# Performance work log

Hardware: AMD Instinct MI355X
Metric: run time of the kernel (lower is better)

The kernel has to match this reference:

```python
import jax, jax.numpy as jnp
import numpy as np

G, B, T, D, U = 3, 32, 1024, 512, 512  # branches, batch, time, feat dim, units

def setup_inputs() -> dict:
    key = jax.random.key(0)
    ks = jax.random.split(key, 8)
    s = 0.02
    return {
        "query": jax.random.normal(ks[0], (G, B, D), jnp.float32),
        "values": jax.random.normal(ks[1], (G, B, T, D), jnp.float32),
        "W1": jax.random.normal(ks[2], (G, D, U), jnp.float32) * s,
        "b1": jnp.zeros((G, U), jnp.float32),
        "W2": jax.random.normal(ks[3], (G, D, U), jnp.float32) * s,
        "b2": jnp.zeros((G, U), jnp.float32),
        "V": jax.random.normal(ks[4], (G, U), jnp.float32) * s,
        "bV": jnp.zeros((G,), jnp.float32),
    }

def reference(query, values, W1, b1, W2, b2, V, bV):
    # query: [G,B,D], values: [G,B,T,D]; G=3 independent additive-attention branches.
    qp = jnp.einsum('gbd,gdu->gbu', query, W1) + b1[:, None, :]          # [G,B,U]
    vp = jnp.einsum('gbtd,gdu->gbtu', values, W2) + b2[:, None, None, :]  # [G,B,T,U]
    feat = jnp.tanh(qp[:, :, None, :] + vp)                               # [G,B,T,U]
    score = jnp.einsum('gbtu,gu->gbt', feat, V) + bV[:, None, None]       # [G,B,T]
    weights = jax.nn.softmax(score, axis=2)                               # softmax over time
    context = jnp.einsum('gbt,gbtd->gbd', weights, values)                # [G,B,D]
    return context, weights[..., None]  # matches tf.stack outputs: [3,B,D], [3,B,T,1]
```

## Files before the change

### kernel.cpp

```cpp
#include <hip/hip_runtime.h>
#include <cstdint>
#include <cstddef>

#define NG 3
#define NB 32
#define NT 1024
#define ND 512
#define NU 512

typedef __bf16 bf16x8 __attribute__((ext_vector_type(8)));
typedef float  f32x16 __attribute__((ext_vector_type(16)));

static __device__ __forceinline__ unsigned int f2bf(float f) {
    union { float f; unsigned int u; } v; v.f = f;
    return (v.u + 0x7FFFu + ((v.u >> 16) & 1u)) >> 16;
}

static __device__ __forceinline__ unsigned int cvt_pk_bf16(float lo, float hi) {
    unsigned int r;
    asm("v_cvt_pk_bf16_f32 %0, %1, %2" : "=v"(r) : "v"(lo), "v"(hi));
    return r;
}

static __device__ __forceinline__ bf16x8 ld_bf16x8(const char* base, int off) {
    return __builtin_bit_cast(bf16x8, *(const uint4*)(base + off));
}

#define AS1(p) ((const __attribute__((address_space(1))) void*)(p))
#define AS3(p) ((__attribute__((address_space(3))) void*)(p))

__global__ __launch_bounds__(256) void prep_qb_kernel(
    const float* __restrict__ query, const float* __restrict__ W1,
    const float* __restrict__ b1, const float* __restrict__ b2,
    float* __restrict__ qb)
{
    __shared__ float qs[NB][ND];
    const int g  = blockIdx.x >> 3;
    const int uc = blockIdx.x & 7;
    const int tid = threadIdx.x;

    const float4* qsrc = (const float4*)(query + (size_t)g * NB * ND);
    #pragma unroll
    for (int i = 0; i < 16; ++i)
        ((float4*)&qs[0][0])[tid + i * 256] = qsrc[tid + i * 256];
    __syncthreads();

    const int u  = uc * 64 + (tid & 63);
    const int b0 = tid >> 6;
    float acc[8] = {};
    const float* w1col = W1 + (size_t)g * ND * NU + u;
    for (int d = 0; d < ND; ++d) {
        float w = w1col[(size_t)d * NU];
        #pragma unroll
        for (int j = 0; j < 8; ++j)
            acc[j] = fmaf(qs[b0 + 4 * j][d], w, acc[j]);
    }
    const float bias = b1[g * NU + u] + b2[g * NU + u];
    #pragma unroll
    for (int j = 0; j < 8; ++j)
        qb[((size_t)g * NB + (b0 + 4 * j)) * NU + u] = acc[j] + bias;
}

__global__ __launch_bounds__(256) void prep_w2t_kernel(
    const float* __restrict__ W2, char* __restrict__ w2t)
{
    __shared__ float tile[64][65];
    const int g  = blockIdx.x >> 6;
    const int tb = blockIdx.x & 63;
    const int d0 = (tb >> 3) * 64;
    const int u0 = (tb & 7) * 64;
    const int tx = threadIdx.x & 63;
    const int ty = threadIdx.x >> 6;

    const float* src = W2 + (size_t)g * ND * NU;
    #pragma unroll
    for (int k = 0; k < 16; ++k) {
        int r = ty + 4 * k;
        tile[r][tx] = src[(size_t)(d0 + r) * NU + (u0 + tx)];
    }
    __syncthreads();
    #pragma unroll
    for (int k = 0; k < 16; ++k) {
        int ul = ty + 4 * k;
        int u  = u0 + ul;
        int d  = d0 + tx;
        unsigned short h = (unsigned short)f2bf(tile[tx][ul]);
        int nb2 = u >> 8, up = u & 255, ksd = d >> 6, kp = d & 63;
        size_t off = ((size_t)((((g << 1) + nb2) << 3) + ksd) << 15)
                   + (size_t)((up << 7) + (((kp << 1) ^ ((up & 7) << 4))));
        *(unsigned short*)(w2t + off) = h;
    }
}

__global__ __launch_bounds__(512, 2) void score_kernel(
    const float* __restrict__ values, const char* __restrict__ w2t,
    const float* __restrict__ qbg, const float* __restrict__ Vvec,
    float* __restrict__ part0, float* __restrict__ part1)
{
    __shared__ char Abuf[2][32768];
    __shared__ char Bbuf[2][32768];
    __shared__ float qbs[256];
    __shared__ float Vs[256];
    __shared__ float spart[4][256];

    const int blk  = blockIdx.x;
    const int g    = blk >> 8;
    const int rr   = blk & 255;
    const int mt   = rr >> 1;
    const int nb   = rr & 1;
    const int b    = mt >> 2;
    const int t0   = (mt & 3) << 8;
    const int tid  = threadIdx.x;
    const int lane = tid & 63;
    const int wave = tid >> 6;
    const int wm   = wave >> 2;
    const int wn   = wave & 3;
    const int rl   = lane & 31;
    const int hi   = lane >> 5;

    const char* bimg = w2t + ((size_t)((((g << 1) + nb) << 3)) << 15);

    if (wave < 4) {
        const float* qsrc = qbg + (((size_t)(g * NB + b)) << 9) + (nb << 8) + (wave << 6) + lane;
        __builtin_amdgcn_global_load_lds(AS1(qsrc), AS3(&qbs[(wave << 6) + lane]), 4, 0, 0);
    } else {
        const float* vsrc = Vvec + (g << 9) + (nb << 8) + ((wave - 4) << 6) + lane;
        __builtin_amdgcn_global_load_lds(AS1(vsrc), AS3(&Vs[((wave - 4) << 6) + lane]), 4, 0, 0);
    }

    auto stageB = [&](int ks, char* dst) {
        const char* src = bimg + ((size_t)ks << 15) + (wave << 12) + (lane << 4);
        char* d = dst + (wave << 12) + (lane << 4);
        #pragma unroll
        for (int i = 0; i < 4; ++i)
            __builtin_amdgcn_global_load_lds(AS1(src + (i << 10)), AS3(d + (i << 10)), 16, 0, 0);
    };

    const int arow  = tid >> 1;
    const int ahalf = tid & 1;
    const float* aptr = values
        + (((size_t)((g * NB + b) * NT + t0 + arow)) << 9) + (ahalf << 5);
    const int awswz = (arow & 7) << 4;

    float4 av[8];
    auto loadA = [&](int ks) {
        const float4* p4 = (const float4*)(aptr + (ks << 6));
        #pragma unroll
        for (int i = 0; i < 8; ++i) av[i] = p4[i];
    };
    auto writeA = [&](char* dst) {
        char* base = dst + (arow << 7);
        #pragma unroll
        for (int q = 0; q < 4; ++q) {
            uint4 w;
            w.x = cvt_pk_bf16(av[2*q].x,   av[2*q].y);
            w.y = cvt_pk_bf16(av[2*q].z,   av[2*q].w);
            w.z = cvt_pk_bf16(av[2*q+1].x, av[2*q+1].y);
            w.w = cvt_pk_bf16(av[2*q+1].z, av[2*q+1].w);
            *(uint4*)(base + (((ahalf << 6) + (q << 4)) ^ awswz)) = w;
        }
    };

    const int lswz = (rl & 7) << 4;
    int koff[4];
    #pragma unroll
    for (int kf = 0; kf < 4; ++kf) koff[kf] = ((kf << 5) + (hi << 4)) ^ lswz;
    const int abase = (((wm << 7) + rl) << 7);
    const int bbase = (((wn << 6) + rl) << 7);

    f32x16 acc[4][2];
    #pragma unroll
    for (int mf = 0; mf < 4; ++mf) {
        acc[mf][0] = (f32x16)(0.0f);
        acc[mf][1] = (f32x16)(0.0f);
    }

    char* Ac = Abuf[0]; char* An = Abuf[1];
    char* Bc = Bbuf[0]; char* Bn = Bbuf[1];

    stageB(0, Bc);
    loadA(0);
    asm volatile("s_waitcnt vmcnt(0) lgkmcnt(0)" ::: "memory");
    writeA(Ac);
    asm volatile("s_waitcnt lgkmcnt(0)" ::: "memory");
    __builtin_amdgcn_s_barrier();

    #pragma unroll 1
    for (int ks = 0; ks < 8; ++ks) {
        if (ks < 7) {
            stageB(ks + 1, Bn);
            loadA(ks + 1);
        }
        __builtin_amdgcn_s_setprio(1);
        #pragma unroll
        for (int kf = 0; kf < 4; ++kf) {
            bf16x8 a0 = ld_bf16x8(Ac, abase         + koff[kf]);
            bf16x8 a1 = ld_bf16x8(Ac, abase +  4096 + koff[kf]);
            bf16x8 a2 = ld_bf16x8(Ac, abase +  8192 + koff[kf]);
            bf16x8 a3 = ld_bf16x8(Ac, abase + 12288 + koff[kf]);
            bf16x8 b0 = ld_bf16x8(Bc, bbase         + koff[kf]);
            bf16x8 b1 = ld_bf16x8(Bc, bbase +  4096 + koff[kf]);
            acc[0][0] = __builtin_amdgcn_mfma_f32_32x32x16_bf16(a0, b0, acc[0][0], 0, 0, 0);
            acc[0][1] = __builtin_amdgcn_mfma_f32_32x32x16_bf16(a0, b1, acc[0][1], 0, 0, 0);
            acc[1][0] = __builtin_amdgcn_mfma_f32_32x32x16_bf16(a1, b0, acc[1][0], 0, 0, 0);
            acc[1][1] = __builtin_amdgcn_mfma_f32_32x32x16_bf16(a1, b1, acc[1][1], 0, 0, 0);
            acc[2][0] = __builtin_amdgcn_mfma_f32_32x32x16_bf16(a2, b0, acc[2][0], 0, 0, 0);
            acc[2][1] = __builtin_amdgcn_mfma_f32_32x32x16_bf16(a2, b1, acc[2][1], 0, 0, 0);
            acc[3][0] = __builtin_amdgcn_mfma_f32_32x32x16_bf16(a3, b0, acc[3][0], 0, 0, 0);
            acc[3][1] = __builtin_amdgcn_mfma_f32_32x32x16_bf16(a3, b1, acc[3][1], 0, 0, 0);
        }
        __builtin_amdgcn_s_setprio(0);
        if (ks < 7) {
            asm volatile("s_waitcnt vmcnt(0)" ::: "memory");
            writeA(An);
            asm volatile("s_waitcnt lgkmcnt(0)" ::: "memory");
            __builtin_amdgcn_s_barrier();
            char* t1 = Ac; Ac = An; An = t1;
            char* t2 = Bc; Bc = Bn; Bn = t2;
        }
    }

    const float qv0 = qbs[(wn << 6) + rl];
    const float qv1 = qbs[(wn << 6) + 32 + rl];
    const float vv0 = Vs[(wn << 6) + rl];
    const float vv1 = Vs[(wn << 6) + 32 + rl];
    const float CL = 2.8853900817779268f;
    #pragma unroll
    for (int mf = 0; mf < 4; ++mf) {
        float p[16];
        #pragma unroll
        for (int r2 = 0; r2 < 16; ++r2) {
            float x0 = acc[mf][0][r2] + qv0;
            float x1 = acc[mf][1][r2] + qv1;
            float e0 = exp2f(CL * x0);
            float e1 = exp2f(CL * x1);
            float th0 = 1.f - 2.f * __builtin_amdgcn_rcpf(e0 + 1.f);
            float th1 = 1.f - 2.f * __builtin_amdgcn_rcpf(e1 + 1.f);
            p[r2] = fmaf(th1, vv1, th0 * vv0);
        }
        #pragma unroll
        for (int r2 = 0; r2 < 16; ++r2) {
            float v = p[r2];
            v += __shfl_xor(v, 1);
            v += __shfl_xor(v, 2);
            v += __shfl_xor(v, 4);
            v += __shfl_xor(v, 8);
            v += __shfl_xor(v, 16);
            p[r2] = v;
        }
        if (rl == 0) {
            #pragma unroll
            for (int r2 = 0; r2 < 16; ++r2)
                spart[wn][(wm << 7) + (mf << 5) + (r2 & 3) + 8 * (r2 >> 2) + 4 * hi] = p[r2];
        }
    }
    __syncthreads();
    if (tid < 256) {
        float s = spart[0][tid] + spart[1][tid] + spart[2][tid] + spart[3][tid];
        float* dst = nb ? part1 : part0;
        dst[(((size_t)(g * NB + b)) << 10) + t0 + tid] = s;
    }
}

__global__ __launch_bounds__(256) void finish_kernel(
    const float* __restrict__ part0, const float* __restrict__ part1,
    const float* __restrict__ bV, const float* __restrict__ values,
    float* __restrict__ out_ctx, float* __restrict__ out_w)
{
    __shared__ float sl[NT];
    __shared__ float red[16];
    __shared__ float cred[4][128];
    const int blk   = blockIdx.x;
    const int gb    = blk >> 2;
    const int slice = blk & 3;
    const int tid = threadIdx.x;
    const int lane = tid & 63, wid = tid >> 6;
    const float bv = bV[gb >> 5];

    float s[4];
    #pragma unroll
    for (int j = 0; j < 4; ++j) {
        int idx = (int)((size_t)gb * NT) + tid + 256 * j;
        s[j] = part0[idx] + part1[idx] + bv;
    }

    float m = fmaxf(fmaxf(s[0], s[1]), fmaxf(s[2], s[3]));
    #pragma unroll
    for (int mask = 32; mask; mask >>= 1) m = fmaxf(m, __shfl_xor(m, mask));
    if (lane == 0) red[wid] = m;
    __syncthreads();
    const float gm = fmaxf(fmaxf(red[0], red[1]), fmaxf(red[2], red[3]));

    float e[4], ps = 0.f;
    #pragma unroll
    for (int j = 0; j < 4; ++j) { e[j] = __expf(s[j] - gm); ps += e[j]; }
    #pragma unroll
    for (int mask = 32; mask; mask >>= 1) ps += __shfl_xor(ps, mask);
    if (lane == 0) red[8 + wid] = ps;
    __syncthreads();
    const float inv = 1.f / (red[8] + red[9] + red[10] + red[11]);

    #pragma unroll
    for (int j = 0; j < 4; ++j) {
        float w = e[j] * inv;
        sl[tid + 256 * j] = w;
        if (slice == 0) out_w[(size_t)gb * NT + tid + 256 * j] = w;
    }
    __syncthreads();

    const int dp = tid & 63;
    const int tg = tid >> 6;
    const float* vbase = values + (size_t)gb * NT * ND + slice * 128 + dp * 2;
    float ax = 0.f, ay = 0.f;
    #pragma unroll 4
    for (int t = tg; t < NT; t += 4) {
        float2 v = *(const float2*)(vbase + (size_t)t * ND);
        float w = sl[t];
        ax = fmaf(w, v.x, ax);
        ay = fmaf(w, v.y, ay);
    }
    cred[tg][dp * 2]     = ax;
    cred[tg][dp * 2 + 1] = ay;
    __syncthreads();
    if (tid < 128) {
        float r = cred[0][tid] + cred[1][tid] + cred[2][tid] + cred[3][tid];
        out_ctx[(size_t)gb * ND + slice * 128 + tid] = r;
    }
}

extern "C" void kernel_launch(void* const* d_in, const int* in_sizes, int n_in,
                              void* d_out, int out_size, void* d_ws, size_t ws_size,
                              hipStream_t stream)
{
    (void)in_sizes; (void)n_in; (void)out_size; (void)ws_size;
    const float* query  = (const float*)d_in[0];
    const float* values = (const float*)d_in[1];
    const float* W1     = (const float*)d_in[2];
    const float* b1     = (const float*)d_in[3];
    const float* W2     = (const float*)d_in[4];
    const float* b2     = (const float*)d_in[5];
    const float* Vv     = (const float*)d_in[6];
    const float* bV     = (const float*)d_in[7];

    float* out_ctx = (float*)d_out;
    float* out_w   = out_ctx + (size_t)NG * NB * ND;

    float* qb    = (float*)d_ws;
    float* part0 = qb + (size_t)NG * NB * NU;
    float* part1 = part0 + (size_t)NG * NB * NT;
    char*  w2t   = (char*)(part1 + (size_t)NG * NB * NT);

    prep_qb_kernel <<<NG * 8,   256, 0, stream>>>(query, W1, b1, b2, qb);
    prep_w2t_kernel<<<NG * 64,  256, 0, stream>>>(W2, w2t);
    score_kernel   <<<NG * 256, 512, 0, stream>>>(values, w2t, qb, Vv, part0, part1);
    finish_kernel  <<<NG * NB * 4, 256, 0, stream>>>(part0, part1, bV, values, out_ctx, out_w);
}
```

Before: 177.7 us.

## Restructure score GEMM main loop into barrier-synchronized phases with deeper A prefetch

Replaces the per-k-step loop with a manually unrolled two-step body split into four phases per k-step. Each phase interleaves one slice of global loads (B staging, half of the A register prefetch, or the A conversion write) with one MFMA cluster, fenced by barriers and sched_barriers. A register prefetch now runs two k-steps ahead using two register sets with partial vmcnt waits, aiming to hide global latency and spread LDS traffic. In exchange it adds more barriers per k-step and raises register pressure under the launch bound of two blocks.

```diff
diff --git a/kernel.cpp b/kernel.cpp
--- a/kernel.cpp
+++ b/kernel.cpp
@@ -92,13 +92,82 @@
     }
 }
 
+#define STAGEB(N_, DST_) do {                                                 \
+    const char* _src = bimg + ((size_t)(N_) << 15) + (wave << 12) + (lane << 4); \
+    char* _d = (DST_) + (wave << 12) + (lane << 4);                           \
+    _Pragma("unroll")                                                         \
+    for (int _i = 0; _i < 4; ++_i)                                            \
+        __builtin_amdgcn_global_load_lds(AS1(_src + (_i << 10)),              \
+                                         AS3(_d + (_i << 10)), 16, 0, 0);     \
+} while (0)
+
+#define LOADA_H(AV_, N_, H_) do {                                             \
+    const float4* _p = (const float4*)(aptr + ((N_) << 6)) + ((H_) << 2);     \
+    _Pragma("unroll")                                                         \
+    for (int _i = 0; _i < 4; ++_i) (AV_)[((H_) << 2) + _i] = _p[_i];          \
+} while (0)
+
+#define WRITEA(AV_, DST_) do {                                                \
+    char* _b = (DST_) + (arow << 7);                                          \
+    _Pragma("unroll")                                                         \
+    for (int _q = 0; _q < 4; ++_q) {                                          \
+        uint4 _w;                                                             \
+        _w.x = cvt_pk_bf16((AV_)[2*_q].x,   (AV_)[2*_q].y);                   \
+        _w.y = cvt_pk_bf16((AV_)[2*_q].z,   (AV_)[2*_q].w);                   \
+        _w.z = cvt_pk_bf16((AV_)[2*_q+1].x, (AV_)[2*_q+1].y);                 \
+        _w.w = cvt_pk_bf16((AV_)[2*_q+1].z, (AV_)[2*_q+1].w);                 \
+        *(uint4*)(_b + (((ahalf << 6) + (_q << 4)) ^ awswz)) = _w;            \
+    }                                                                         \
+} while (0)
+
+#define MFMA8(A0_,A1_,A2_,A3_,B0_,B1_) do {                                   \
+    acc[0][0] = __builtin_amdgcn_mfma_f32_32x32x16_bf16(A0_, B0_, acc[0][0], 0, 0, 0); \
+    acc[0][1] = __builtin_amdgcn_mfma_f32_32x32x16_bf16(A0_, B1_, acc[0][1], 0, 0, 0); \
+    acc[1][0] = __builtin_amdgcn_mfma_f32_32x32x16_bf16(A1_, B0_, acc[1][0], 0, 0, 0); \
+    acc[1][1] = __builtin_amdgcn_mfma_f32_32x32x16_bf16(A1_, B1_, acc[1][1], 0, 0, 0); \
+    acc[2][0] = __builtin_amdgcn_mfma_f32_32x32x16_bf16(A2_, B0_, acc[2][0], 0, 0, 0); \
+    acc[2][1] = __builtin_amdgcn_mfma_f32_32x32x16_bf16(A2_, B1_, acc[2][1], 0, 0, 0); \
+    acc[3][0] = __builtin_amdgcn_mfma_f32_32x32x16_bf16(A3_, B0_, acc[3][0], 0, 0, 0); \
+    acc[3][1] = __builtin_amdgcn_mfma_f32_32x32x16_bf16(A3_, B1_, acc[3][1], 0, 0, 0); \
+} while (0)
+
+#define PHASE(ARD_, BRD_, KOFF_, EXTRA_) do {                                 \
+    bf16x8 _a0 = ld_bf16x8((ARD_), abase         + (KOFF_));                  \
+    bf16x8 _a1 = ld_bf16x8((ARD_), abase +  4096 + (KOFF_));                  \
+    bf16x8 _a2 = ld_bf16x8((ARD_), abase +  8192 + (KOFF_));                  \
+    bf16x8 _a3 = ld_bf16x8((ARD_), abase + 12288 + (KOFF_));                  \
+    bf16x8 _b0 = ld_bf16x8((BRD_), bbase         + (KOFF_));                  \
+    bf16x8 _b1 = ld_bf16x8((BRD_), bbase +  4096 + (KOFF_));                  \
+    EXTRA_;                                                                   \
+    __builtin_amdgcn_s_barrier();                                             \
+    asm volatile("s_waitcnt lgkmcnt(0)" ::: "memory");                        \
+    __builtin_amdgcn_sched_barrier(0);                                        \
+    __builtin_amdgcn_s_setprio(1);                                            \
+    MFMA8(_a0, _a1, _a2, _a3, _b0, _b1);                                      \
+    __builtin_amdgcn_s_setprio(0);                                            \
+    __builtin_amdgcn_s_barrier();                                             \
+} while (0)
+
+#define BODY(KS_, AVL_, AVW_, ARD_, AWR_, BRD_, BWR_) do {                    \
+    PHASE(ARD_, BRD_, koff0, if ((KS_) < 7) STAGEB((KS_) + 1, BWR_));         \
+    PHASE(ARD_, BRD_, koff1, if ((KS_) < 6) LOADA_H(AVL_, (KS_) + 2, 0));     \
+    PHASE(ARD_, BRD_, koff2, if ((KS_) < 6) LOADA_H(AVL_, (KS_) + 2, 1));     \
+    PHASE(ARD_, BRD_, koff3,                                                  \
+        if ((KS_) < 7) {                                                      \
+            if ((KS_) < 6) { asm volatile("s_waitcnt vmcnt(8)" ::: "memory"); } \
+            else           { asm volatile("s_waitcnt vmcnt(0)" ::: "memory"); } \
+            __builtin_amdgcn_sched_barrier(0);                                \
+            WRITEA(AVW_, AWR_);                                               \
+        });                                                                   \
+} while (0)
+
 __global__ __launch_bounds__(512, 2) void score_kernel(
     const float* __restrict__ values, const char* __restrict__ w2t,
     const float* __restrict__ qbg, const float* __restrict__ Vvec,
     float* __restrict__ part0, float* __restrict__ part1)
 {
-    __shared__ char Abuf[2][32768];
-    __shared__ char Bbuf[2][32768];
+    __shared__ char Ab0[32768], Ab1[32768];
+    __shared__ char Bb0[32768], Bb1[32768];
     __shared__ float qbs[256];
     __shared__ float Vs[256];
     __shared__ float spart[4][256];
@@ -128,43 +197,28 @@
         __builtin_amdgcn_global_load_lds(AS1(vsrc), AS3(&Vs[((wave - 4) << 6) + lane]), 4, 0, 0);
     }
 
-    auto stageB = [&](int ks, char* dst) {
-        const char* src = bimg + ((size_t)ks << 15) + (wave << 12) + (lane << 4);
-        char* d = dst + (wave << 12) + (lane << 4);
-        #pragma unroll
-        for (int i = 0; i < 4; ++i)
-            __builtin_amdgcn_global_load_lds(AS1(src + (i << 10)), AS3(d + (i << 10)), 16, 0, 0);
-    };
-
     const int arow  = tid >> 1;
     const int ahalf = tid & 1;
     const float* aptr = values
         + (((size_t)((g * NB + b) * NT + t0 + arow)) << 9) + (ahalf << 5);
     const int awswz = (arow & 7) << 4;
 
-    float4 av[8];
-    auto loadA = [&](int ks) {
-        const float4* p4 = (const float4*)(aptr + (ks << 6));
-        #pragma unroll
-        for (int i = 0; i < 8; ++i) av[i] = p4[i];
-    };
-    auto writeA = [&](char* dst) {
-        char* base = dst + (arow << 7);
-        #pragma unroll
-        for (int q = 0; q < 4; ++q) {
-            uint4 w;
-            w.x = cvt_pk_bf16(av[2*q].x,   av[2*q].y);
-            w.y = cvt_pk_bf16(av[2*q].z,   av[2*q].w);
-            w.z = cvt_pk_bf16(av[2*q+1].x, av[2*q+1].y);
-            w.w = cvt_pk_bf16(av[2*q+1].z, av[2*q+1].w);
-            *(uint4*)(base + (((ahalf << 6) + (q << 4)) ^ awswz)) = w;
-        }
-    };
-
-    const int lswz = (rl & 7) << 4;
-    int koff[4];
-    #pragma unroll
-    for (int kf = 0; kf < 4; ++kf) koff[kf] = ((kf << 5) + (hi << 4)) ^ lswz;
+    STAGEB(0, Bb0);
+    float4 av0[8], av1[8];
+    LOADA_H(av0, 0, 0); LOADA_H(av0, 0, 1);
+    LOADA_H(av1, 1, 0); LOADA_H(av1, 1, 1);
+    asm volatile("s_waitcnt vmcnt(8)" ::: "memory");
+    __builtin_amdgcn_sched_barrier(0);
+    WRITEA(av0, Ab0);
+    asm volatile("s_waitcnt lgkmcnt(0)" ::: "memory");
+    __builtin_amdgcn_sched_barrier(0);
+    __builtin_amdgcn_s_barrier();
+
+    const int lswz  = (rl & 7) << 4;
+    const int koff0 = ((0 << 5) + (hi << 4)) ^ lswz;
+    const int koff1 = ((1 << 5) + (hi << 4)) ^ lswz;
+    const int koff2 = ((2 << 5) + (hi << 4)) ^ lswz;
+    const int koff3 = ((3 << 5) + (hi << 4)) ^ lswz;
     const int abase = (((wm << 7) + rl) << 7);
     const int bbase = (((wn << 6) + rl) << 7);
 
@@ -175,49 +229,10 @@
         acc[mf][1] = (f32x16)(0.0f);
     }
 
-    char* Ac = Abuf[0]; char* An = Abuf[1];
-    char* Bc = Bbuf[0]; char* Bn = Bbuf[1];
-
-    stageB(0, Bc);
-    loadA(0);
-    asm volatile("s_waitcnt vmcnt(0) lgkmcnt(0)" ::: "memory");
-    writeA(Ac);
-    asm volatile("s_waitcnt lgkmcnt(0)" ::: "memory");
-    __builtin_amdgcn_s_barrier();
-
     #pragma unroll 1
-    for (int ks = 0; ks < 8; ++ks) {
-        if (ks < 7) {
-            stageB(ks + 1, Bn);
-            loadA(ks + 1);
-        }
-        __builtin_amdgcn_s_setprio(1);
-        #pragma unroll
-        for (int kf = 0; kf < 4; ++kf) {
-            bf16x8 a0 = ld_bf16x8(Ac, abase         + koff[kf]);
-            bf16x8 a1 = ld_bf16x8(Ac, abase +  4096 + koff[kf]);
-            bf16x8 a2 = ld_bf16x8(Ac, abase +  8192 + koff[kf]);
-            bf16x8 a3 = ld_bf16x8(Ac, abase + 12288 + koff[kf]);
-            bf16x8 b0 = ld_bf16x8(Bc, bbase         + koff[kf]);
-            bf16x8 b1 = ld_bf16x8(Bc, bbase +  4096 + koff[kf]);
-            acc[0][0] = __builtin_amdgcn_mfma_f32_32x32x16_bf16(a0, b0, acc[0][0], 0, 0, 0);
-            acc[0][1] = __builtin_amdgcn_mfma_f32_32x32x16_bf16(a0, b1, acc[0][1], 0, 0, 0);
-            acc[1][0] = __builtin_amdgcn_mfma_f32_32x32x16_bf16(a1, b0, acc[1][0], 0, 0, 0);
-            acc[1][1] = __builtin_amdgcn_mfma_f32_32x32x16_bf16(a1, b1, acc[1][1], 0, 0, 0);
-            acc[2][0] = __builtin_amdgcn_mfma_f32_32x32x16_bf16(a2, b0, acc[2][0], 0, 0, 0);
-            acc[2][1] = __builtin_amdgcn_mfma_f32_32x32x16_bf16(a2, b1, acc[2][1], 0, 0, 0);
-            acc[3][0] = __builtin_amdgcn_mfma_f32_32x32x16_bf16(a3, b0, acc[3][0], 0, 0, 0);
-            acc[3][1] = __builtin_amdgcn_mfma_f32_32x32x16_bf16(a3, b1, acc[3][1], 0, 0, 0);
-        }
-        __builtin_amdgcn_s_setprio(0);
-        if (ks < 7) {
-            asm volatile("s_waitcnt vmcnt(0)" ::: "memory");
-            writeA(An);
-            asm volatile("s_waitcnt lgkmcnt(0)" ::: "memory");
-            __builtin_amdgcn_s_barrier();
-            char* t1 = Ac; Ac = An; An = t1;
-            char* t2 = Bc; Bc = Bn; Bn = t2;
-        }
+    for (int ks = 0; ks < 8; ks += 2) {
+        BODY(ks,     av0, av1, Ab0, Ab1, Bb0, Bb1);
+        BODY(ks + 1, av1, av0, Ab1, Ab0, Bb1, Bb0);
     }
 
     const float qv0 = qbs[(wn << 6) + rl];
```

After: 186.4 us. 1.05x slower.
